# Performance work log

Measured on AMD Instinct MI355X. Metric: run time of the kernel, lower is better.

The kernel has to match this reference:

```python
import jax, jax.numpy as jnp
import numpy as np
import math

B, L, DM, DI, DS, DR, K, NL = 1, 1024, 768, 1536, 16, 48, 4, 2
DT_MIN, DT_MAX = 0.001, 0.1


def rmsnorm(x, w, eps=1e-5):
    return x * jax.lax.rsqrt(jnp.mean(x * x, axis=-1, keepdims=True) + eps) * w


def causal_dwconv(x, w, b):
    # x: [B,L,C], w: [C,1,K]. torch Conv1d(padding=K-1)[..., :L] == left-pad K-1 causal conv.
    y = jax.lax.conv_general_dilated(
        x.transpose(0, 2, 1), w, (1,), [(K - 1, 0)],
        dimension_numbers=('NCH', 'OIH', 'NCH'), feature_group_count=DI)
    return y.transpose(0, 2, 1) + b


def selective_scan(x, delta, A, Bm, Cm, D):
    # x, delta: [B,L,DI]; A: [DI,DS]; Bm, Cm: [B,L,DS]; D: [DI]
    dA = jnp.exp(delta[..., None] * A)               # [B,L,DI,DS]
    BX = (delta * x)[..., None] * Bm[:, :, None, :]  # [B,L,DI,DS]

    def comb(c1, c2):
        a1, b1 = c1
        a2, b2 = c2
        return (a1 * a2, a2 * b1 + b2)

    _, hs = jax.lax.associative_scan(comb, (dA, BX), axis=1)  # h_t = dA_t*h_{t-1} + BX_t
    return jnp.einsum('bldn,bln->bld', hs, Cm) + D * x


def ssm(x, xproj_w, dt_w, dt_b, A_log, D):
    dbc = jnp.einsum('bld,ed->ble', x, xproj_w)            # [B,L,DR+2*DS]
    dlt, Bm, Cm = jnp.split(dbc, [DR, DR + DS], axis=-1)
    delta = jax.nn.softplus(jnp.einsum('blr,dr->bld', dlt, dt_w) + dt_b)
    return selective_scan(x, delta, -jnp.exp(A_log), Bm, Cm, D)


def mamba_block(x, p):
    xz = jnp.einsum('bld,ed->ble', x, p['in_w'])           # [B,L,2*DI]
    xin, z = jnp.split(xz, 2, axis=-1)
    xf = jax.nn.silu(causal_dwconv(xin, p['cf_w'], p['cf_b']))
    xb = jax.nn.silu(causal_dwconv(xin[:, ::-1, :], p['cb_w'], p['cb_b']))
    yf = ssm(xf, p['xf_w'], p['dtf_w'], p['dtf_b'], p['Af'], p['Df'])
    yb = ssm(xb, p['xb_w'], p['dtb_w'], p['dtb_b'], p['Ab'], p['Db'])  # NOT flipped back (faithful)
    y = jnp.einsum('ble,de->bld', jnp.concatenate([yf, yb], axis=-1), p['pro_w']) + p['pro_b']
    # tokenizer: scores over L, softmax along L, mix values; dropout = identity (eval)
    att = jax.nn.softmax(jnp.einsum('bld,td->btl', y, p['wA']), axis=-1)  # [B,T=L,L]
    vv = jnp.einsum('bld,de->ble', y, p['wV'])
    y = jnp.einsum('btl,ble->bte', att, vv)
    return jnp.einsum('bld,od->blo', y * jax.nn.silu(z), p['out_w'])


def reference(x, norm_w, in_proj_w, conv_f_w, conv_f_b, conv_b_w, conv_b_b,
              xproj_f_w, xproj_b_w, dt_f_w, dt_f_b, dt_b_w, dt_b_b,
              A_log_f, D_f, A_log_b, D_b, out_w, token_wA, token_wV, pro_w, pro_b):
    for i in range(NL):
        p = dict(in_w=in_proj_w[i], cf_w=conv_f_w[i], cf_b=conv_f_b[i],
                 cb_w=conv_b_w[i], cb_b=conv_b_b[i], xf_w=xproj_f_w[i],
                 xb_w=xproj_b_w[i], dtf_w=dt_f_w[i], dtf_b=dt_f_b[i],
                 dtb_w=dt_b_w[i], dtb_b=dt_b_b[i], Af=A_log_f[i], Df=D_f[i],
                 Ab=A_log_b[i], Db=D_b[i], out_w=out_w[i], wA=token_wA[i],
                 wV=token_wV[i], pro_w=pro_w[i], pro_b=pro_b[i])
        x = x + mamba_block(rmsnorm(x, norm_w[i]), p)
    return x


def setup_inputs():
    key = jax.random.key(0)
    ks = jax.random.split(key, 16)
    rn = lambda k, sh, s=0.02: jax.random.normal(k, sh, jnp.float32) * s
    A_log = jnp.broadcast_to(jnp.log(jnp.arange(1, DS + 1, dtype=jnp.float32)), (NL, DI, DS))
    dt = jnp.exp(jax.random.uniform(ks[0], (NL, DI)) * (math.log(DT_MAX) - math.log(DT_MIN)) + math.log(DT_MIN))
    inv_dt = dt + jnp.log(-jnp.expm1(-dt))  # softplus^-1(dt)
    dt_std = DR ** -0.5
    kaiming = (2.0 / DI) ** 0.5
    return {
        'x': jax.random.normal(ks[1], (B, L, DM), jnp.float32),
        'norm_w': jnp.ones((NL, DM), jnp.float32),
        'in_proj_w': rn(ks[2], (NL, 2 * DI, DM)),
        'conv_f_w': rn(ks[3], (NL, DI, 1, K), 0.3),
        'conv_f_b': jnp.zeros((NL, DI), jnp.float32),
        'conv_b_w': rn(ks[4], (NL, DI, 1, K), 0.3),
        'conv_b_b': jnp.zeros((NL, DI), jnp.float32),
        'xproj_f_w': rn(ks[5], (NL, DR + 2 * DS, DI)),
        'xproj_b_w': rn(ks[6], (NL, DR + 2 * DS, DI)),
        'dt_f_w': jax.random.uniform(ks[7], (NL, DI, DR), jnp.float32, -dt_std, dt_std),
        'dt_f_b': inv_dt,
        'dt_b_w': jax.random.uniform(ks[8], (NL, DI, DR), jnp.float32, -dt_std, dt_std),
        'dt_b_b': inv_dt,
        'A_log_f': A_log,
        'D_f': jnp.ones((NL, DI), jnp.float32),
        'A_log_b': A_log,
        'D_b': jnp.ones((NL, DI), jnp.float32),
        'out_w': rn(ks[9], (NL, DM, DI)),
        'token_wA': rn(ks[10], (NL, L, DI), kaiming),
        'token_wV': rn(ks[11], (NL, DI, DI), kaiming),
        'pro_w': rn(ks[12], (NL, DI, 2 * DI)),
        'pro_b': jnp.zeros((NL, DI), jnp.float32),
    }
```

## Files before the change

kernel.cpp:

```cpp
#include <hip/hip_runtime.h>
#include <hip/hip_bf16.h>
#include <math.h>
#include <stdint.h>

#define LSEQ 1024
#define DMODEL 768
#define DINNER 1536
#define DSTATE 16
#define DRANK 48
#define KCONV 4
#define NLAYER 2
#define DBC 80
#define NQ 4
#define QL (LSEQ / NQ)
#define QCH (QL / 16)

typedef unsigned short u16;
typedef __attribute__((ext_vector_type(8))) __bf16 bf16x8;
typedef __attribute__((ext_vector_type(4))) float f32x4;
typedef __attribute__((ext_vector_type(4))) unsigned short us4;

__device__ __forceinline__ u16 f2bf(float f) {
  union { float f; unsigned u; } v; v.f = f;
  unsigned r = v.u + 0x7fffu + ((v.u >> 16) & 1u);
  return (u16)(r >> 16);
}

__device__ __forceinline__ void gload16(const void* g, void* l) {
  auto gp = reinterpret_cast<const __attribute__((address_space(1))) uint32_t*>(
      reinterpret_cast<uintptr_t>(g));
  auto lp = reinterpret_cast<__attribute__((address_space(3))) uint32_t*>(
      reinterpret_cast<uintptr_t>(l));
  __builtin_amdgcn_global_load_lds(gp, lp, 16, 0, 0);
}

__global__ __launch_bounds__(256) void cvt_k(const float* __restrict__ in,
                                             u16* __restrict__ out, int n4) {
  int i = blockIdx.x * 256 + threadIdx.x;
  if (i >= n4) return;
  float4 v = ((const float4*)in)[i];
  us4 o; o[0] = f2bf(v.x); o[1] = f2bf(v.y); o[2] = f2bf(v.z); o[3] = f2bf(v.w);
  ((us4*)out)[i] = o;
}

__global__ __launch_bounds__(256) void transcvt_k(const float* __restrict__ in,
                                                  u16* __restrict__ out,
                                                  int R, int C) {
  __shared__ float t[32][33];
  int c0 = blockIdx.x * 32, r0 = blockIdx.y * 32;
  int tx = threadIdx.x & 31, ty = threadIdx.x >> 5;
  for (int i = ty; i < 32; i += 8) t[i][tx] = in[(size_t)(r0 + i) * C + c0 + tx];
  __syncthreads();
  for (int i = ty; i < 32; i += 8)
    out[(size_t)(c0 + i) * R + r0 + tx] = f2bf(t[tx][i]);
}

__global__ __launch_bounds__(256) void transpose16_k(const u16* __restrict__ in,
                                                     u16* __restrict__ out,
                                                     int R, int C) {
  __shared__ u16 t[32][34];
  int c0 = blockIdx.x * 32, r0 = blockIdx.y * 32;
  int tx = threadIdx.x & 31, ty = threadIdx.x >> 5;
  for (int i = ty; i < 32; i += 8) t[i][tx] = in[(size_t)(r0 + i) * C + c0 + tx];
  __syncthreads();
  for (int i = ty; i < 32; i += 8)
    out[(size_t)(c0 + i) * R + r0 + tx] = t[tx][i];
}

__global__ __launch_bounds__(256) void rmsnorm_k(const float* __restrict__ x,
                                                 const float* __restrict__ w,
                                                 u16* __restrict__ xn) {
  int row = blockIdx.x;
  int tid = threadIdx.x;
  const float* xr = x + (size_t)row * DMODEL;
  float ss = 0.f;
  for (int j = tid; j < DMODEL; j += 256) { float v = xr[j]; ss += v * v; }
  __shared__ float red[256];
  red[tid] = ss; __syncthreads();
  for (int s = 128; s > 0; s >>= 1) { if (tid < s) red[tid] += red[tid + s]; __syncthreads(); }
  float scale = rsqrtf(red[0] / (float)DMODEL + 1e-5f);
  u16* outr = xn + (size_t)row * DMODEL;
  for (int j = tid; j < DMODEL; j += 256) outr[j] = f2bf(xr[j] * scale * w[j]);
}

template<int EPI>
__global__ __launch_bounds__(256) void mgemm_k(
    const u16* __restrict__ A, int lda,
    const u16* __restrict__ B, int ldb,
    void* __restrict__ Cv, int ldc, int K,
    const float* __restrict__ bias,
    const float* __restrict__ resid, int ldr)
{
  __shared__ u16 As[2][64 * 64];
  __shared__ u16 Bs[2][64 * 64];
  const int tid = threadIdx.x;
  const int lane = tid & 63;
  const int w = tid >> 6;

  const int nbx = gridDim.x;
  int bid = blockIdx.y * nbx + blockIdx.x;
  const int nwg = nbx * gridDim.y;
  bid = (bid & 7) * (nwg >> 3) + (bid >> 3);
  const int bm = (bid / nbx) * 64;
  const int bn = (bid % nbx) * 64;

  const int srow = lane >> 3;
  const int scs = (lane & 7) ^ srow;
  const int gA = 2 * w;
  const u16* Asrc0 = A + (size_t)(bm + gA * 8 + srow) * lda + scs * 8;
  const u16* Asrc1 = Asrc0 + (size_t)8 * lda;
  const u16* Bsrc0 = B + (size_t)(bn + gA * 8 + srow) * ldb + scs * 8;
  const u16* Bsrc1 = Bsrc0 + (size_t)8 * ldb;
  const int d0 = gA * 512;
  const int d1 = d0 + 512;

  const int fr = lane & 15;
  const int fs = lane >> 4;
  const int wm = (w >> 1) * 32;
  const int wn = (w & 1) * 32;
  int aoff[2][2], boff[2][2];
#pragma unroll
  for (int i = 0; i < 2; i++)
#pragma unroll
    for (int h = 0; h < 2; h++) {
      const int g = h * 4 + fs;
      aoff[i][h] = (wm + i * 16 + fr) * 64 + (g ^ (fr & 7)) * 8;
      boff[i][h] = (wn + i * 16 + fr) * 64 + (g ^ (fr & 7)) * 8;
    }

  f32x4 acc[2][2];
#pragma unroll
  for (int i = 0; i < 2; i++)
#pragma unroll
    for (int j = 0; j < 2; j++) acc[i][j] = (f32x4){0.f, 0.f, 0.f, 0.f};

#define STAGE(buf, k0) do { \
    gload16(Asrc0 + (k0), &As[buf][d0]); \
    gload16(Asrc1 + (k0), &As[buf][d1]); \
    gload16(Bsrc0 + (k0), &Bs[buf][d0]); \
    gload16(Bsrc1 + (k0), &Bs[buf][d1]); \
  } while (0)

  const int nk = K >> 6;
  STAGE(0, 0);

  for (int t = 0; t < nk; t++) {
    const int buf = t & 1;
    __syncthreads();
    if (t + 1 < nk) STAGE(buf ^ 1, (t + 1) << 6);
    const u16* As_ = As[buf];
    const u16* Bs_ = Bs[buf];
#pragma unroll
    for (int h = 0; h < 2; h++) {
      bf16x8 a0 = *reinterpret_cast<const bf16x8*>(As_ + aoff[0][h]);
      bf16x8 a1 = *reinterpret_cast<const bf16x8*>(As_ + aoff[1][h]);
      bf16x8 b0 = *reinterpret_cast<const bf16x8*>(Bs_ + boff[0][h]);
      bf16x8 b1 = *reinterpret_cast<const bf16x8*>(Bs_ + boff[1][h]);
      acc[0][0] = __builtin_amdgcn_mfma_f32_16x16x32_bf16(a0, b0, acc[0][0], 0, 0, 0);
      acc[0][1] = __builtin_amdgcn_mfma_f32_16x16x32_bf16(a0, b1, acc[0][1], 0, 0, 0);
      acc[1][0] = __builtin_amdgcn_mfma_f32_16x16x32_bf16(a1, b0, acc[1][0], 0, 0, 0);
      acc[1][1] = __builtin_amdgcn_mfma_f32_16x16x32_bf16(a1, b1, acc[1][1], 0, 0, 0);
    }
  }
#undef STAGE

#pragma unroll
  for (int i = 0; i < 2; i++) {
#pragma unroll
    for (int j = 0; j < 2; j++) {
      const int col = bn + wn + j * 16 + fr;
      const int row0 = bm + wm + i * 16 + fs * 4;
      float bv = (EPI & 1) ? bias[col] : 0.f;
#pragma unroll
      for (int r = 0; r < 4; r++) {
        float v = acc[i][j][r] + bv;
        if (EPI & 4) v += resid[(size_t)(row0 + r) * ldr + col];
        if (EPI & 16) {
          float z = resid[(size_t)(row0 + r) * ldr + col];
          v *= z / (1.f + __expf(-z));
        }
        if (EPI & 8) ((u16*)Cv)[(size_t)(row0 + r) * ldc + col] = f2bf(v);
        else         ((float*)Cv)[(size_t)(row0 + r) * ldc + col] = v;
      }
    }
  }
}

#define TG_R 16
#define TG_KC 96
#define TG_KS 16

__global__ __launch_bounds__(256) void thin_gemm_k(
    const float* __restrict__ Af_, const float* __restrict__ Ab_,
    const float* __restrict__ Bf_, const float* __restrict__ Bb_,
    float* __restrict__ partial)
{
  __shared__ float As[TG_R][100];
  __shared__ float Bs[80][100];
  const float* A = blockIdx.z ? Ab_ : Af_;
  const float* B = blockIdx.z ? Bb_ : Bf_;
  float* part = partial + (size_t)blockIdx.z * TG_KS * LSEQ * DBC;
  const int tid = threadIdx.x;
  const int m0 = blockIdx.x * TG_R;
  const int ks = blockIdx.y;
  const int k0 = ks * TG_KC;

  for (int i = tid; i < 384; i += 256) {
    int r = i / 24, q = i % 24;
    *(float4*)&As[r][q * 4] = *(const float4*)(A + (size_t)(m0 + r) * DINNER + k0 + q * 4);
  }
  for (int i = tid; i < 1920; i += 256) {
    int r = i / 24, q = i % 24;
    *(float4*)&Bs[r][q * 4] = *(const float4*)(B + (size_t)r * DINNER + k0 + q * 4);
  }
  __syncthreads();

  const int r = tid >> 4;
  const int c0 = (tid & 15) * 5;
  float acc[5] = {};
  for (int k = 0; k < TG_KC; k++) {
    float a = As[r][k];
#pragma unroll
    for (int j = 0; j < 5; j++) acc[j] += a * Bs[c0 + j][k];
  }
  float* out = part + ((size_t)ks * LSEQ + m0 + r) * DBC + c0;
#pragma unroll
  for (int j = 0; j < 5; j++) out[j] = acc[j];
}

__global__ __launch_bounds__(256) void reduce_dbc_k(const float* __restrict__ partial,
                                                    float* __restrict__ outf,
                                                    float* __restrict__ outb) {
  int i = blockIdx.x * 256 + threadIdx.x;
  const float* part = partial + (size_t)blockIdx.y * TG_KS * LSEQ * DBC;
  float s = 0.f;
#pragma unroll
  for (int ks = 0; ks < TG_KS; ks++) s += part[(size_t)ks * (LSEQ * DBC) + i];
  (blockIdx.y ? outb : outf)[i] = s;
}

#define BM 64
#define BN 64
#define BK 16

__global__ __launch_bounds__(256) void delta_gemm_k(
    const float* __restrict__ A0, const float* __restrict__ A1,
    const float* __restrict__ B0, const float* __restrict__ B1,
    const float* __restrict__ b0, const float* __restrict__ b1,
    float* __restrict__ C0, float* __restrict__ C1)
{
  __shared__ float Asf[BK][BM];
  __shared__ float Bsf[BK][BN + 4];
  const float* A = blockIdx.z ? A1 : A0;
  const float* B = blockIdx.z ? B1 : B0;
  const float* bias = blockIdx.z ? b1 : b0;
  float* C = blockIdx.z ? C1 : C0;
  const int tid = threadIdx.x;
  const int bm = blockIdx.y * BM;
  const int bn = blockIdx.x * BN;
  const int ar = tid >> 2;
  const int ak = (tid & 3) << 2;
  const int ty = tid >> 4, tx = tid & 15;
  float acc[4][4] = {};

  for (int k0 = 0; k0 < DRANK; k0 += BK) {
    float4 av = *(const float4*)(A + (size_t)(bm + ar) * DBC + k0 + ak);
    float4 bv = *(const float4*)(B + (size_t)(bn + ar) * DRANK + k0 + ak);
    __syncthreads();
    Asf[ak + 0][ar] = av.x; Asf[ak + 1][ar] = av.y;
    Asf[ak + 2][ar] = av.z; Asf[ak + 3][ar] = av.w;
    Bsf[ak + 0][ar] = bv.x; Bsf[ak + 1][ar] = bv.y;
    Bsf[ak + 2][ar] = bv.z; Bsf[ak + 3][ar] = bv.w;
    __syncthreads();
#pragma unroll
    for (int kk = 0; kk < BK; kk++) {
      float4 a4 = *(const float4*)&Asf[kk][ty * 4];
      float4 b4 = *(const float4*)&Bsf[kk][tx * 4];
      float a[4] = {a4.x, a4.y, a4.z, a4.w};
      float b[4] = {b4.x, b4.y, b4.z, b4.w};
#pragma unroll
      for (int i = 0; i < 4; i++)
#pragma unroll
        for (int j = 0; j < 4; j++)
          acc[i][j] += a[i] * b[j];
    }
  }

#pragma unroll
  for (int i = 0; i < 4; i++) {
    int row = bm + ty * 4 + i;
#pragma unroll
    for (int j = 0; j < 4; j++) {
      int col = bn + tx * 4 + j;
      float v = acc[i][j] + bias[col];
      v = (v > 20.f) ? v : log1pf(__expf(v));
      C[(size_t)row * DINNER + col] = v;
    }
  }
}

__global__ __launch_bounds__(256) void conv_silu_k(
    const float* __restrict__ xz,
    const float* __restrict__ wf, const float* __restrict__ bf,
    const float* __restrict__ wb, const float* __restrict__ bb,
    float* __restrict__ xf, float* __restrict__ xb)
{
  int idx = blockIdx.x * 256 + threadIdx.x;
  int dir = blockIdx.y;
  if (idx >= LSEQ * DINNER) return;
  int l = idx / DINNER, c = idx % DINNER;
  const float* w = (dir ? wb : wf) + c * KCONV;
  float acc = (dir ? bb : bf)[c];
#pragma unroll
  for (int k = 0; k < KCONV; k++) {
    int ls = l - (KCONV - 1) + k;
    if (ls >= 0) {
      int lsrc = dir ? (LSEQ - 1 - ls) : ls;
      acc += w[k] * xz[(size_t)lsrc * (2 * DINNER) + c];
    }
  }
  float sv = acc / (1.f + __expf(-acc));
  (dir ? xb : xf)[idx] = sv;
}


__global__ __launch_bounds__(256) void scan_a_k(
    const float* __restrict__ xcf, const float* __restrict__ xcb,
    const float* __restrict__ dltf, const float* __restrict__ dltb,
    const float* __restrict__ dbcf, const float* __restrict__ dbcb,
    const float* __restrict__ Af, const float* __restrict__ Ab,
    float* __restrict__ qsP, float* __restrict__ qsQ)
{
  __shared__ float sP[16 * 16 * 16];
  __shared__ float sQ[16 * 16 * 16];
  const int dir = blockIdx.z;
  const int qid = blockIdx.y;
  const float* xc    = dir ? xcb : xcf;
  const float* delta = dir ? dltb : dltf;
  const float* dbc   = dir ? dbcb : dbcf;
  const float* A_log = dir ? Ab : Af;

  const int tid = threadIdx.x;
  const int c = tid >> 4;
  const int dl = tid & 15;
  const int d = blockIdx.x * 16 + dl;

  float Aa[DSTATE];
#pragma unroll
  for (int s = 0; s < DSTATE; s++) Aa[s] = -__expf(A_log[(size_t)d * DSTATE + s]);

  float aP[DSTATE], q[DSTATE];
#pragma unroll
  for (int s = 0; s < DSTATE; s++) { aP[s] = 1.f; q[s] = 0.f; }
  const int l0 = qid * QL + c * QCH;
  for (int i = 0; i < QCH; i++) {
    int l = l0 + i;
    float dt = delta[(size_t)l * DINNER + d];
    float dx = dt * xc[(size_t)l * DINNER + d];
    const float* bm = dbc + (size_t)l * DBC + DRANK;
#pragma unroll
    for (int s = 0; s < DSTATE; s++) {
      float a = __expf(dt * Aa[s]);
      q[s] = a * q[s] + dx * bm[s];
      aP[s] *= a;
    }
  }
#pragma unroll
  for (int s = 0; s < DSTATE; s++) {
    sP[(c * 16 + dl) * 16 + s] = aP[s];
    sQ[(c * 16 + dl) * 16 + s] = q[s];
  }
  __syncthreads();

  {
    const int d2 = tid >> 4, s2 = tid & 15;
    float h = 0.f, P = 1.f;
    for (int cc = 0; cc < 16; cc++) {
      int idx = (cc * 16 + d2) * 16 + s2;
      float a = sP[idx];
      h = a * h + sQ[idx];
      P *= a;
    }
    size_t o = (((size_t)dir * NQ + qid) * DINNER + blockIdx.x * 16 + d2) * 16 + s2;
    qsP[o] = P;
    qsQ[o] = h;
  }
}

__global__ __launch_bounds__(256) void scan_b_k(const float* __restrict__ qsP,
                                                const float* __restrict__ qsQ,
                                                float* __restrict__ carry) {
  int i = blockIdx.x * 256 + threadIdx.x;
  int dir = i / (DINNER * DSTATE);
  int rem = i % (DINNER * DSTATE);
  float h = 0.f;
#pragma unroll
  for (int q = 0; q < NQ; q++) {
    size_t o = ((size_t)dir * NQ + q) * (DINNER * DSTATE) + rem;
    carry[o] = h;
    h = qsP[o] * h + qsQ[o];
  }
}

__global__ __launch_bounds__(256) void scan_c_k(
    const float* __restrict__ xcf, const float* __restrict__ xcb,
    const float* __restrict__ dltf, const float* __restrict__ dltb,
    const float* __restrict__ dbcf, const float* __restrict__ dbcb,
    const float* __restrict__ Af, const float* __restrict__ Ab,
    const float* __restrict__ Df, const float* __restrict__ Db,
    const float* __restrict__ carry,
    u16* __restrict__ ycat)
{
  __shared__ float sP[16 * 16 * 16];
  __shared__ float sQ[16 * 16 * 16];
  const int dir = blockIdx.z;
  const int qid = blockIdx.y;
  const float* xc    = dir ? xcb : xcf;
  const float* delta = dir ? dltb : dltf;
  const float* dbc   = dir ? dbcb : dbcf;
  const float* A_log = dir ? Ab : Af;
  const float* Dvec  = dir ? Db : Df;
  const int col_off  = dir ? DINNER : 0;

  const int tid = threadIdx.x;
  const int c = tid >> 4;
  const int dl = tid & 15;
  const int d = blockIdx.x * 16 + dl;

  float Aa[DSTATE];
#pragma unroll
  for (int s = 0; s < DSTATE; s++) Aa[s] = -__expf(A_log[(size_t)d * DSTATE + s]);

  float aP[DSTATE], q[DSTATE];
#pragma unroll
  for (int s = 0; s < DSTATE; s++) { aP[s] = 1.f; q[s] = 0.f; }
  const int l0 = qid * QL + c * QCH;
  for (int i = 0; i < QCH; i++) {
    int l = l0 + i;
    float dt = delta[(size_t)l * DINNER + d];
    float dx = dt * xc[(size_t)l * DINNER + d];
    const float* bm = dbc + (size_t)l * DBC + DRANK;
#pragma unroll
    for (int s = 0; s < DSTATE; s++) {
      float a = __expf(dt * Aa[s]);
      q[s] = a * q[s] + dx * bm[s];
      aP[s] *= a;
    }
  }
#pragma unroll
  for (int s = 0; s < DSTATE; s++) {
    sP[(c * 16 + dl) * 16 + s] = aP[s];
    sQ[(c * 16 + dl) * 16 + s] = q[s];
  }
  __syncthreads();

  {
    const int d2 = tid >> 4, s2 = tid & 15;
    float h = carry[(((size_t)dir * NQ + qid) * DINNER + blockIdx.x * 16 + d2) * 16 + s2];
    for (int cc = 0; cc < 16; cc++) {
      int idx = (cc * 16 + d2) * 16 + s2;
      float a = sP[idx], qq = sQ[idx];
      sP[idx] = h;
      h = a * h + qq;
    }
  }
  __syncthreads();

  float hs[DSTATE];
#pragma unroll
  for (int s = 0; s < DSTATE; s++) hs[s] = sP[(c * 16 + dl) * 16 + s];
  const float Dd = Dvec[d];
  for (int i = 0; i < QCH; i++) {
    int l = l0 + i;
    float dt = delta[(size_t)l * DINNER + d];
    float xv = xc[(size_t)l * DINNER + d];
    float dx = dt * xv;
    const float* bm = dbc + (size_t)l * DBC + DRANK;
    const float* cm = bm + DSTATE;
    float y = 0.f;
#pragma unroll
    for (int s = 0; s < DSTATE; s++) {
      float a = __expf(dt * Aa[s]);
      hs[s] = a * hs[s] + dx * bm[s];
      y += hs[s] * cm[s];
    }
    ycat[(size_t)l * (2 * DINNER) + col_off + d] = f2bf(y + Dd * xv);
  }
}

__global__ __launch_bounds__(256) void softmax_k(const float* __restrict__ S,
                                                 u16* __restrict__ P) {
  int row = blockIdx.x, tid = threadIdx.x;
  __shared__ float buf[LSEQ];
  __shared__ float red[256];
  const float* r = S + (size_t)row * LSEQ;
  float m = -1e30f;
  for (int j = tid; j < LSEQ; j += 256) { float v = r[j]; buf[j] = v; m = fmaxf(m, v); }
  red[tid] = m; __syncthreads();
  for (int s = 128; s > 0; s >>= 1) { if (tid < s) red[tid] = fmaxf(red[tid], red[tid + s]); __syncthreads(); }
  m = red[0];
  __syncthreads();
  float sum = 0.f;
  for (int j = tid; j < LSEQ; j += 256) { float e = __expf(buf[j] - m); buf[j] = e; sum += e; }
  red[tid] = sum; __syncthreads();
  for (int s = 128; s > 0; s >>= 1) { if (tid < s) red[tid] += red[tid + s]; __syncthreads(); }
  float inv = 1.f / red[0];
  u16* pr = P + (size_t)row * LSEQ;
  for (int j = tid; j < LSEQ; j += 256) pr[j] = f2bf(buf[j] * inv);
}

extern "C" void kernel_launch(void* const* d_in, const int* in_sizes, int n_in,
                              void* d_out, int out_size, void* d_ws, size_t ws_size,
                              hipStream_t stream) {
  const float* in_x      = (const float*)d_in[0];
  const float* norm_w    = (const float*)d_in[1];
  const float* in_proj_w = (const float*)d_in[2];
  const float* conv_f_w  = (const float*)d_in[3];
  const float* conv_f_b  = (const float*)d_in[4];
  const float* conv_b_w  = (const float*)d_in[5];
  const float* conv_b_b  = (const float*)d_in[6];
  const float* xproj_f_w = (const float*)d_in[7];
  const float* xproj_b_w = (const float*)d_in[8];
  const float* dt_f_w    = (const float*)d_in[9];
  const float* dt_f_b    = (const float*)d_in[10];
  const float* dt_b_w    = (const float*)d_in[11];
  const float* dt_b_b    = (const float*)d_in[12];
  const float* A_log_f   = (const float*)d_in[13];
  const float* D_f       = (const float*)d_in[14];
  const float* A_log_b   = (const float*)d_in[15];
  const float* D_b       = (const float*)d_in[16];
  const float* out_w     = (const float*)d_in[17];
  const float* token_wA  = (const float*)d_in[18];
  const float* token_wV  = (const float*)d_in[19];
  const float* pro_w     = (const float*)d_in[20];
  const float* pro_b     = (const float*)d_in[21];

  float* ws = (float*)d_ws;
  float* xbuf = ws; ws += LSEQ * DMODEL;
  float* xz   = ws; ws += LSEQ * 2 * DINNER;
  float* xf   = ws; ws += LSEQ * DINNER;
  float* xb   = ws; ws += LSEQ * DINNER;
  float* dbcf = ws; ws += LSEQ * DBC;
  float* dbcb = ws; ws += LSEQ * DBC;
  float* delf = ws; ws += LSEQ * DINNER;
  float* delb = ws; ws += LSEQ * DINNER;
  float* scr  = ws; ws += LSEQ * DINNER;
  u16* xn_bf   = (u16*)ws; ws += (LSEQ * DMODEL) / 2;
  u16* ycat_bf = (u16*)ws; ws += LSEQ * DINNER;
  u16* ypro_bf = (u16*)ws; ws += (LSEQ * DINNER) / 2;
  u16* Wb      = (u16*)ws;
  u16* in_w_bf = Wb;
  u16* pw_bf   = in_w_bf + 3072 * 768;
  u16* wA_bf   = pw_bf + 1536 * 3072;
  u16* wVT_bf  = wA_bf + 1024 * 1536;
  u16* ow_bf   = wVT_bf + 1536 * 1536;

  float* dbc_part = delf;
  float* Smat    = delf;
  u16*   Smat_bf = (u16*)delb;
  u16*   vv_bf   = (u16*)xf;
  u16*   vvT_bf  = (u16*)xb;
  u16*   g_bf    = ypro_bf;
  const int QS = 2 * NQ * DINNER * DSTATE;
  float* qsP   = scr;
  float* qsQ   = scr + QS;
  float* qcar  = scr + 2 * QS;

  hipMemcpyAsync(xbuf, in_x, sizeof(float) * LSEQ * DMODEL,
                 hipMemcpyDeviceToDevice, stream);

  dim3 blk(256);
  for (int layer = 0; layer < NLAYER; layer++) {
    const float* nw  = norm_w    + (size_t)layer * DMODEL;
    const float* iw  = in_proj_w + (size_t)layer * 2 * DINNER * DMODEL;
    const float* cfw = conv_f_w  + (size_t)layer * DINNER * KCONV;
    const float* cfb = conv_f_b  + (size_t)layer * DINNER;
    const float* cbw = conv_b_w  + (size_t)layer * DINNER * KCONV;
    const float* cbb = conv_b_b  + (size_t)layer * DINNER;
    const float* xfw = xproj_f_w + (size_t)layer * DBC * DINNER;
    const float* xbw = xproj_b_w + (size_t)layer * DBC * DINNER;
    const float* dfw = dt_f_w    + (size_t)layer * DINNER * DRANK;
    const float* dfb = dt_f_b    + (size_t)layer * DINNER;
    const float* dbw = dt_b_w    + (size_t)layer * DINNER * DRANK;
    const float* dbb = dt_b_b    + (size_t)layer * DINNER;
    const float* Af  = A_log_f   + (size_t)layer * DINNER * DSTATE;
    const float* Df  = D_f       + (size_t)layer * DINNER;
    const float* Ab  = A_log_b   + (size_t)layer * DINNER * DSTATE;
    const float* Db  = D_b       + (size_t)layer * DINNER;
    const float* ow  = out_w     + (size_t)layer * DMODEL * DINNER;
    const float* wA  = token_wA  + (size_t)layer * LSEQ * DINNER;
    const float* wV  = token_wV  + (size_t)layer * DINNER * DINNER;
    const float* pw  = pro_w     + (size_t)layer * DINNER * 2 * DINNER;
    const float* pb  = pro_b     + (size_t)layer * DINNER;

    cvt_k<<<(3072 * 768 / 4 + 255) / 256, blk, 0, stream>>>(iw, in_w_bf, 3072 * 768 / 4);
    cvt_k<<<(1536 * 3072 / 4 + 255) / 256, blk, 0, stream>>>(pw, pw_bf, 1536 * 3072 / 4);
    cvt_k<<<(1024 * 1536 / 4 + 255) / 256, blk, 0, stream>>>(wA, wA_bf, 1024 * 1536 / 4);
    cvt_k<<<(768 * 1536 / 4 + 255) / 256, blk, 0, stream>>>(ow, ow_bf, 768 * 1536 / 4);
    transcvt_k<<<dim3(1536 / 32, 1536 / 32), blk, 0, stream>>>(wV, wVT_bf, 1536, 1536);

    rmsnorm_k<<<LSEQ, blk, 0, stream>>>(xbuf, nw, xn_bf);

    mgemm_k<0><<<dim3(3072 / 64, LSEQ / 64), blk, 0, stream>>>(
        xn_bf, DMODEL, in_w_bf, DMODEL, xz, 2 * DINNER, DMODEL, nullptr, nullptr, 0);

    conv_silu_k<<<dim3((LSEQ * DINNER) / 256, 2), blk, 0, stream>>>(
        xz, cfw, cfb, cbw, cbb, xf, xb);

    thin_gemm_k<<<dim3(LSEQ / TG_R, TG_KS, 2), blk, 0, stream>>>(
        xf, xb, xfw, xbw, dbc_part);
    reduce_dbc_k<<<dim3((LSEQ * DBC) / 256, 2), blk, 0, stream>>>(
        dbc_part, dbcf, dbcb);

    delta_gemm_k<<<dim3(DINNER / BN, LSEQ / BM, 2), blk, 0, stream>>>(
        dbcf, dbcb, dfw, dbw, dfb, dbb, delf, delb);

    scan_a_k<<<dim3(DINNER / 16, NQ, 2), blk, 0, stream>>>(
        xf, xb, delf, delb, dbcf, dbcb, Af, Ab, qsP, qsQ);
    scan_b_k<<<(2 * DINNER * DSTATE) / 256, blk, 0, stream>>>(qsP, qsQ, qcar);
    scan_c_k<<<dim3(DINNER / 16, NQ, 2), blk, 0, stream>>>(
        xf, xb, delf, delb, dbcf, dbcb, Af, Ab, Df, Db, qcar, ycat_bf);

    mgemm_k<9><<<dim3(DINNER / 64, LSEQ / 64), blk, 0, stream>>>(
        ycat_bf, 2 * DINNER, pw_bf, 2 * DINNER, ypro_bf, DINNER, 2 * DINNER,
        pb, nullptr, 0);

    mgemm_k<0><<<dim3(LSEQ / 64, LSEQ / 64), blk, 0, stream>>>(
        wA_bf, DINNER, ypro_bf, DINNER, Smat, LSEQ, DINNER, nullptr, nullptr, 0);
    softmax_k<<<LSEQ, blk, 0, stream>>>(Smat, Smat_bf);

    mgemm_k<8><<<dim3(DINNER / 64, LSEQ / 64), blk, 0, stream>>>(
        ypro_bf, DINNER, wVT_bf, DINNER, vv_bf, DINNER, DINNER, nullptr, nullptr, 0);

    transpose16_k<<<dim3(DINNER / 32, LSEQ / 32), blk, 0, stream>>>(
        vv_bf, vvT_bf, LSEQ, DINNER);

    mgemm_k<24><<<dim3(DINNER / 64, LSEQ / 64), blk, 0, stream>>>(
        Smat_bf, LSEQ, vvT_bf, LSEQ, g_bf, DINNER, LSEQ,
        nullptr, xz + DINNER, 2 * DINNER);

    float* target = (layer == NLAYER - 1) ? (float*)d_out : xbuf;
    mgemm_k<4><<<dim3(DMODEL / 64, LSEQ / 64), blk, 0, stream>>>(
        g_bf, DINNER, ow_bf, DINNER, target, DMODEL, DINNER,
        nullptr, xbuf, DMODEL);
  }
}
```

Measured before the change: 459.6 us.

## Merge launches: fuse weight casts, S/V GEMMs, scan carry; store delta as bf16

Folds the four weight-cast launches into one kernel and the two independent token GEMMs (scores and values) into one grouped launch of 640 blocks. It also drops the separate carry-scan kernel by having each scan_c block recompute its prefix carry from the chunk summaries, and writes delta in bf16 to halve its traffic. The initial device-to-device input copy is removed by reading the input directly in layer 0. Together these cut launch count and memory traffic, at the cost of lower precision for delta and some redundant carry work in scan_c.

```diff
diff --git a/kernel.cpp b/kernel.cpp
--- a/kernel.cpp
+++ b/kernel.cpp
@@ -25,6 +25,10 @@
   unsigned r = v.u + 0x7fffu + ((v.u >> 16) & 1u);
   return (u16)(r >> 16);
 }
+__device__ __forceinline__ float bf2f(u16 u) {
+  union { unsigned u; float f; } v; v.u = ((unsigned)u) << 16;
+  return v.f;
+}
 
 __device__ __forceinline__ void gload16(const void* g, void* l) {
   auto gp = reinterpret_cast<const __attribute__((address_space(1))) uint32_t*>(
@@ -34,13 +38,24 @@
   __builtin_amdgcn_global_load_lds(gp, lp, 16, 0, 0);
 }
 
-__global__ __launch_bounds__(256) void cvt_k(const float* __restrict__ in,
-                                             u16* __restrict__ out, int n4) {
+#define CV0 589824
+#define CV1 (CV0 + 1179648)
+#define CV2 (CV1 + 393216)
+#define CV3 (CV2 + 294912)
+__global__ __launch_bounds__(256) void cvt4_k(
+    const float* __restrict__ i0, u16* __restrict__ o0,
+    const float* __restrict__ i1, u16* __restrict__ o1,
+    const float* __restrict__ i2, u16* __restrict__ o2,
+    const float* __restrict__ i3, u16* __restrict__ o3) {
   int i = blockIdx.x * 256 + threadIdx.x;
-  if (i >= n4) return;
-  float4 v = ((const float4*)in)[i];
+  const float* in; u16* out; int off;
+  if (i < CV0)      { in = i0; out = o0; off = i; }
+  else if (i < CV1) { in = i1; out = o1; off = i - CV0; }
+  else if (i < CV2) { in = i2; out = o2; off = i - CV1; }
+  else              { in = i3; out = o3; off = i - CV2; }
+  float4 v = ((const float4*)in)[off];
   us4 o; o[0] = f2bf(v.x); o[1] = f2bf(v.y); o[2] = f2bf(v.z); o[3] = f2bf(v.w);
-  ((us4*)out)[i] = o;
+  ((us4*)out)[off] = o;
 }
 
 __global__ __launch_bounds__(256) void transcvt_k(const float* __restrict__ in,
@@ -186,6 +201,100 @@
   }
 }
 
+__global__ __launch_bounds__(256) void svgemm_k(
+    const u16* __restrict__ wA, const u16* __restrict__ ypro,
+    const u16* __restrict__ wVT,
+    float* __restrict__ Smat, u16* __restrict__ vv)
+{
+  __shared__ u16 As[2][64 * 64];
+  __shared__ u16 Bs[2][64 * 64];
+  const int tid = threadIdx.x;
+  const int lane = tid & 63;
+  const int w = tid >> 6;
+
+  int bid = blockIdx.x;
+  bid = (bid & 7) * 80 + (bid >> 3);
+  const bool is_s = bid < 256;
+  const u16* A;
+  const u16* B;
+  int bm, bn;
+  if (is_s) { A = wA;   B = ypro; bm = (bid >> 4) * 64;         bn = (bid & 15) * 64; }
+  else      { A = ypro; B = wVT;  bm = ((bid - 256) / 24) * 64; bn = ((bid - 256) % 24) * 64; }
+
+  const int srow = lane >> 3;
+  const int scs = (lane & 7) ^ srow;
+  const int gA = 2 * w;
+  const u16* Asrc0 = A + (size_t)(bm + gA * 8 + srow) * DINNER + scs * 8;
+  const u16* Asrc1 = Asrc0 + (size_t)8 * DINNER;
+  const u16* Bsrc0 = B + (size_t)(bn + gA * 8 + srow) * DINNER + scs * 8;
+  const u16* Bsrc1 = Bsrc0 + (size_t)8 * DINNER;
+  const int d0 = gA * 512;
+  const int d1 = d0 + 512;
+
+  const int fr = lane & 15;
+  const int fs = lane >> 4;
+  const int wm = (w >> 1) * 32;
+  const int wn = (w & 1) * 32;
+  int aoff[2][2], boff[2][2];
+#pragma unroll
+  for (int i = 0; i < 2; i++)
+#pragma unroll
+    for (int h = 0; h < 2; h++) {
+      const int g = h * 4 + fs;
+      aoff[i][h] = (wm + i * 16 + fr) * 64 + (g ^ (fr & 7)) * 8;
+      boff[i][h] = (wn + i * 16 + fr) * 64 + (g ^ (fr & 7)) * 8;
+    }
+
+  f32x4 acc[2][2];
+#pragma unroll
+  for (int i = 0; i < 2; i++)
+#pragma unroll
+    for (int j = 0; j < 2; j++) acc[i][j] = (f32x4){0.f, 0.f, 0.f, 0.f};
+
+#define STAGE(buf, k0) do { \
+    gload16(Asrc0 + (k0), &As[buf][d0]); \
+    gload16(Asrc1 + (k0), &As[buf][d1]); \
+    gload16(Bsrc0 + (k0), &Bs[buf][d0]); \
+    gload16(Bsrc1 + (k0), &Bs[buf][d1]); \
+  } while (0)
+
+  STAGE(0, 0);
+  for (int t = 0; t < DINNER / 64; t++) {
+    const int buf = t & 1;
+    __syncthreads();
+    if (t + 1 < DINNER / 64) STAGE(buf ^ 1, (t + 1) << 6);
+    const u16* As_ = As[buf];
+    const u16* Bs_ = Bs[buf];
+#pragma unroll
+    for (int h = 0; h < 2; h++) {
+      bf16x8 a0 = *reinterpret_cast<const bf16x8*>(As_ + aoff[0][h]);
+      bf16x8 a1 = *reinterpret_cast<const bf16x8*>(As_ + aoff[1][h]);
+      bf16x8 b0 = *reinterpret_cast<const bf16x8*>(Bs_ + boff[0][h]);
+      bf16x8 b1 = *reinterpret_cast<const bf16x8*>(Bs_ + boff[1][h]);
+      acc[0][0] = __builtin_amdgcn_mfma_f32_16x16x32_bf16(a0, b0, acc[0][0], 0, 0, 0);
+      acc[0][1] = __builtin_amdgcn_mfma_f32_16x16x32_bf16(a0, b1, acc[0][1], 0, 0, 0);
+      acc[1][0] = __builtin_amdgcn_mfma_f32_16x16x32_bf16(a1, b0, acc[1][0], 0, 0, 0);
+      acc[1][1] = __builtin_amdgcn_mfma_f32_16x16x32_bf16(a1, b1, acc[1][1], 0, 0, 0);
+    }
+  }
+#undef STAGE
+
+#pragma unroll
+  for (int i = 0; i < 2; i++) {
+#pragma unroll
+    for (int j = 0; j < 2; j++) {
+      const int col = bn + wn + j * 16 + fr;
+      const int row0 = bm + wm + i * 16 + fs * 4;
+#pragma unroll
+      for (int r = 0; r < 4; r++) {
+        float v = acc[i][j][r];
+        if (is_s) Smat[(size_t)(row0 + r) * LSEQ + col] = v;
+        else      vv[(size_t)(row0 + r) * DINNER + col] = f2bf(v);
+      }
+    }
+  }
+}
+
 #define TG_R 16
 #define TG_KC 96
 #define TG_KS 16
@@ -247,14 +356,14 @@
     const float* __restrict__ A0, const float* __restrict__ A1,
     const float* __restrict__ B0, const float* __restrict__ B1,
     const float* __restrict__ b0, const float* __restrict__ b1,
-    float* __restrict__ C0, float* __restrict__ C1)
+    u16* __restrict__ C0, u16* __restrict__ C1)
 {
   __shared__ float Asf[BK][BM];
   __shared__ float Bsf[BK][BN + 4];
   const float* A = blockIdx.z ? A1 : A0;
   const float* B = blockIdx.z ? B1 : B0;
   const float* bias = blockIdx.z ? b1 : b0;
-  float* C = blockIdx.z ? C1 : C0;
+  u16* C = blockIdx.z ? C1 : C0;
   const int tid = threadIdx.x;
   const int bm = blockIdx.y * BM;
   const int bn = blockIdx.x * BN;
@@ -294,7 +403,7 @@
       int col = bn + tx * 4 + j;
       float v = acc[i][j] + bias[col];
       v = (v > 20.f) ? v : log1pf(__expf(v));
-      C[(size_t)row * DINNER + col] = v;
+      C[(size_t)row * DINNER + col] = f2bf(v);
     }
   }
 }
@@ -323,10 +432,9 @@
   (dir ? xb : xf)[idx] = sv;
 }
 
-
 __global__ __launch_bounds__(256) void scan_a_k(
     const float* __restrict__ xcf, const float* __restrict__ xcb,
-    const float* __restrict__ dltf, const float* __restrict__ dltb,
+    const u16* __restrict__ dltf, const u16* __restrict__ dltb,
     const float* __restrict__ dbcf, const float* __restrict__ dbcb,
     const float* __restrict__ Af, const float* __restrict__ Ab,
     float* __restrict__ qsP, float* __restrict__ qsQ)
@@ -336,7 +444,7 @@
   const int dir = blockIdx.z;
   const int qid = blockIdx.y;
   const float* xc    = dir ? xcb : xcf;
-  const float* delta = dir ? dltb : dltf;
+  const u16*   delta = dir ? dltb : dltf;
   const float* dbc   = dir ? dbcb : dbcf;
   const float* A_log = dir ? Ab : Af;
 
@@ -355,7 +463,7 @@
   const int l0 = qid * QL + c * QCH;
   for (int i = 0; i < QCH; i++) {
     int l = l0 + i;
-    float dt = delta[(size_t)l * DINNER + d];
+    float dt = bf2f(delta[(size_t)l * DINNER + d]);
     float dx = dt * xc[(size_t)l * DINNER + d];
     const float* bm = dbc + (size_t)l * DBC + DRANK;
 #pragma unroll
@@ -387,28 +495,13 @@
   }
 }
 
-__global__ __launch_bounds__(256) void scan_b_k(const float* __restrict__ qsP,
-                                                const float* __restrict__ qsQ,
-                                                float* __restrict__ carry) {
-  int i = blockIdx.x * 256 + threadIdx.x;
-  int dir = i / (DINNER * DSTATE);
-  int rem = i % (DINNER * DSTATE);
-  float h = 0.f;
-#pragma unroll
-  for (int q = 0; q < NQ; q++) {
-    size_t o = ((size_t)dir * NQ + q) * (DINNER * DSTATE) + rem;
-    carry[o] = h;
-    h = qsP[o] * h + qsQ[o];
-  }
-}
-
 __global__ __launch_bounds__(256) void scan_c_k(
     const float* __restrict__ xcf, const float* __restrict__ xcb,
-    const float* __restrict__ dltf, const float* __restrict__ dltb,
+    const u16* __restrict__ dltf, const u16* __restrict__ dltb,
     const float* __restrict__ dbcf, const float* __restrict__ dbcb,
     const float* __restrict__ Af, const float* __restrict__ Ab,
     const float* __restrict__ Df, const float* __restrict__ Db,
-    const float* __restrict__ carry,
+    const float* __restrict__ qsP, const float* __restrict__ qsQ,
     u16* __restrict__ ycat)
 {
   __shared__ float sP[16 * 16 * 16];
@@ -416,7 +509,7 @@
   const int dir = blockIdx.z;
   const int qid = blockIdx.y;
   const float* xc    = dir ? xcb : xcf;
-  const float* delta = dir ? dltb : dltf;
+  const u16*   delta = dir ? dltb : dltf;
   const float* dbc   = dir ? dbcb : dbcf;
   const float* A_log = dir ? Ab : Af;
   const float* Dvec  = dir ? Db : Df;
@@ -437,7 +530,7 @@
   const int l0 = qid * QL + c * QCH;
   for (int i = 0; i < QCH; i++) {
     int l = l0 + i;
-    float dt = delta[(size_t)l * DINNER + d];
+    float dt = bf2f(delta[(size_t)l * DINNER + d]);
     float dx = dt * xc[(size_t)l * DINNER + d];
     const float* bm = dbc + (size_t)l * DBC + DRANK;
 #pragma unroll
@@ -456,7 +549,12 @@
 
   {
     const int d2 = tid >> 4, s2 = tid & 15;
-    float h = carry[(((size_t)dir * NQ + qid) * DINNER + blockIdx.x * 16 + d2) * 16 + s2];
+    size_t base = ((size_t)dir * NQ * DINNER + blockIdx.x * 16 + d2) * 16 + s2;
+    float h = 0.f;
+    for (int qq = 0; qq < qid; qq++) {
+      size_t o = base + (size_t)qq * DINNER * 16;
+      h = qsP[o] * h + qsQ[o];
+    }
     for (int cc = 0; cc < 16; cc++) {
       int idx = (cc * 16 + d2) * 16 + s2;
       float a = sP[idx], qq = sQ[idx];
@@ -472,7 +570,7 @@
   const float Dd = Dvec[d];
   for (int i = 0; i < QCH; i++) {
     int l = l0 + i;
-    float dt = delta[(size_t)l * DINNER + d];
+    float dt = bf2f(delta[(size_t)l * DINNER + d]);
     float xv = xc[(size_t)l * DINNER + d];
     float dx = dt * xv;
     const float* bm = dbc + (size_t)l * DBC + DRANK;
@@ -542,8 +640,8 @@
   float* xb   = ws; ws += LSEQ * DINNER;
   float* dbcf = ws; ws += LSEQ * DBC;
   float* dbcb = ws; ws += LSEQ * DBC;
-  float* delf = ws; ws += LSEQ * DINNER;
-  float* delb = ws; ws += LSEQ * DINNER;
+  float* delf_r = ws; ws += LSEQ * DINNER;
+  float* delb_r = ws; ws += LSEQ * DINNER;
   float* scr  = ws; ws += LSEQ * DINNER;
   u16* xn_bf   = (u16*)ws; ws += (LSEQ * DMODEL) / 2;
   u16* ycat_bf = (u16*)ws; ws += LSEQ * DINNER;
@@ -555,19 +653,17 @@
   u16* wVT_bf  = wA_bf + 1024 * 1536;
   u16* ow_bf   = wVT_bf + 1536 * 1536;
 
-  float* dbc_part = delf;
-  float* Smat    = delf;
-  u16*   Smat_bf = (u16*)delb;
-  u16*   vv_bf   = (u16*)xf;
-  u16*   vvT_bf  = (u16*)xb;
-  u16*   g_bf    = ypro_bf;
+  float* dbc_part = delf_r;
+  u16*   delf_bf  = (u16*)delf_r;
+  u16*   delb_bf  = (u16*)delb_r;
+  float* Smat     = delf_r;
+  u16*   Smat_bf  = (u16*)delb_r;
+  u16*   vv_bf    = (u16*)xf;
+  u16*   vvT_bf   = (u16*)xb;
+  u16*   g_bf     = ypro_bf;
   const int QS = 2 * NQ * DINNER * DSTATE;
   float* qsP   = scr;
   float* qsQ   = scr + QS;
-  float* qcar  = scr + 2 * QS;
-
-  hipMemcpyAsync(xbuf, in_x, sizeof(float) * LSEQ * DMODEL,
-                 hipMemcpyDeviceToDevice, stream);
 
   dim3 blk(256);
   for (int layer = 0; layer < NLAYER; layer++) {
@@ -593,13 +689,12 @@
     const float* pw  = pro_w     + (size_t)layer * DINNER * 2 * DINNER;
     const float* pb  = pro_b     + (size_t)layer * DINNER;
 
-    cvt_k<<<(3072 * 768 / 4 + 255) / 256, blk, 0, stream>>>(iw, in_w_bf, 3072 * 768 / 4);
-    cvt_k<<<(1536 * 3072 / 4 + 255) / 256, blk, 0, stream>>>(pw, pw_bf, 1536 * 3072 / 4);
-    cvt_k<<<(1024 * 1536 / 4 + 255) / 256, blk, 0, stream>>>(wA, wA_bf, 1024 * 1536 / 4);
-    cvt_k<<<(768 * 1536 / 4 + 255) / 256, blk, 0, stream>>>(ow, ow_bf, 768 * 1536 / 4);
+    const float* xsrc = (layer == 0) ? in_x : xbuf;
+
+    cvt4_k<<<CV3 / 256, blk, 0, stream>>>(iw, in_w_bf, pw, pw_bf, wA, wA_bf, ow, ow_bf);
     transcvt_k<<<dim3(1536 / 32, 1536 / 32), blk, 0, stream>>>(wV, wVT_bf, 1536, 1536);
 
-    rmsnorm_k<<<LSEQ, blk, 0, stream>>>(xbuf, nw, xn_bf);
+    rmsnorm_k<<<LSEQ, blk, 0, stream>>>(xsrc, nw, xn_bf);
 
     mgemm_k<0><<<dim3(3072 / 64, LSEQ / 64), blk, 0, stream>>>(
         xn_bf, DMODEL, in_w_bf, DMODEL, xz, 2 * DINNER, DMODEL, nullptr, nullptr, 0);
@@ -613,24 +708,19 @@
         dbc_part, dbcf, dbcb);
 
     delta_gemm_k<<<dim3(DINNER / BN, LSEQ / BM, 2), blk, 0, stream>>>(
-        dbcf, dbcb, dfw, dbw, dfb, dbb, delf, delb);
+        dbcf, dbcb, dfw, dbw, dfb, dbb, delf_bf, delb_bf);
 
     scan_a_k<<<dim3(DINNER / 16, NQ, 2), blk, 0, stream>>>(
-        xf, xb, delf, delb, dbcf, dbcb, Af, Ab, qsP, qsQ);
-    scan_b_k<<<(2 * DINNER * DSTATE) / 256, blk, 0, stream>>>(qsP, qsQ, qcar);
+        xf, xb, delf_bf, delb_bf, dbcf, dbcb, Af, Ab, qsP, qsQ);
     scan_c_k<<<dim3(DINNER / 16, NQ, 2), blk, 0, stream>>>(
-        xf, xb, delf, delb, dbcf, dbcb, Af, Ab, Df, Db, qcar, ycat_bf);
+        xf, xb, delf_bf, delb_bf, dbcf, dbcb, Af, Ab, Df, Db, qsP, qsQ, ycat_bf);
 
     mgemm_k<9><<<dim3(DINNER / 64, LSEQ / 64), blk, 0, stream>>>(
         ycat_bf, 2 * DINNER, pw_bf, 2 * DINNER, ypro_bf, DINNER, 2 * DINNER,
         pb, nullptr, 0);
 
-    mgemm_k<0><<<dim3(LSEQ / 64, LSEQ / 64), blk, 0, stream>>>(
-        wA_bf, DINNER, ypro_bf, DINNER, Smat, LSEQ, DINNER, nullptr, nullptr, 0);
+    svgemm_k<<<640, blk, 0, stream>>>(wA_bf, ypro_bf, wVT_bf, Smat, vv_bf);
     softmax_k<<<LSEQ, blk, 0, stream>>>(Smat, Smat_bf);
-
-    mgemm_k<8><<<dim3(DINNER / 64, LSEQ / 64), blk, 0, stream>>>(
-        ypro_bf, DINNER, wVT_bf, DINNER, vv_bf, DINNER, DINNER, nullptr, nullptr, 0);
 
     transpose16_k<<<dim3(DINNER / 32, LSEQ / 32), blk, 0, stream>>>(
         vv_bf, vvT_bf, LSEQ, DINNER);
@@ -642,6 +732,6 @@
     float* target = (layer == NLAYER - 1) ? (float*)d_out : xbuf;
     mgemm_k<4><<<dim3(DMODEL / 64, LSEQ / 64), blk, 0, stream>>>(
         g_bf, DINNER, ow_bf, DINNER, target, DMODEL, DINNER,
-        nullptr, xbuf, DMODEL);
-  }
-}
+        nullptr, xsrc, DMODEL);
+  }
+}
```

Measured after the change: 423.5 us. 1.09x faster.
